# Kernel tuning notes

Hardware: AMD Instinct MI355X
Metric: run time of the kernel (lower is better)

## Reference

```python
import jax, jax.numpy as jnp
import numpy as np

EPS = 1e-5

def _ste(x, q):
    # straight-through estimator: forward = q, backward = identity
    return x + jax.lax.stop_gradient(q - x)

def quant_act_int4(x):
    # per-token absmax quantization to int4 range [-8, 7] (dequantized)
    s = jnp.clip(jnp.max(jnp.abs(x), axis=-1, keepdims=True), EPS, None) / 7.0
    q = jnp.clip(jnp.round(x / s), -8.0, 7.0) * s
    return _ste(x, q)

def ternary_weight(w):
    # absmean ternary quantization: scale = mean(|w|), w_q in {-1,0,+1} * scale
    scale = jnp.clip(jnp.mean(jnp.abs(w)), EPS, None)
    t = jnp.clip(jnp.round(w / scale), -1.0, 1.0)
    return _ste(w, t * scale)

def setup_inputs() -> dict:
    key = jax.random.key(0)
    kx, kw = jax.random.split(key)
    in_features, out_features = 4096, 16384
    x = jax.random.normal(kx, (4, 2048, in_features), dtype=jnp.float32)
    # kaiming_uniform_(a=sqrt(5)) -> U(-b, b), b = sqrt(6/((1+5)*fan_in)) = 1/sqrt(fan_in)
    bound = 1.0 / np.sqrt(in_features)
    latent_weight = jax.random.uniform(kw, (out_features, in_features), dtype=jnp.float32,
                                       minval=-bound, maxval=bound)
    return {"x": x, "latent_weight": latent_weight}

def reference(x, latent_weight):
    xq = quant_act_int4(x)                    # (B, S, in)
    w_eff = ternary_weight(latent_weight)     # (out, in)
    return jnp.einsum('bsi,oi->bso', xq, w_eff)
```

## Files before the change

### kernel.cpp

```cpp
#include <hip/hip_runtime.h>
#include <hip/hip_bf16.h>
#include <stdint.h>


#define K_DIM 4096
#define M_DIM 8192
#define N_DIM 16384

typedef int v4i __attribute__((ext_vector_type(4)));

typedef __attribute__((address_space(1))) void gvoid_t;
typedef __attribute__((address_space(3))) void lvoid_t;

__device__ __forceinline__ void gl_lds16(const void* g, void* l) {
    __builtin_amdgcn_global_load_lds((gvoid_t*)(void*)g, (lvoid_t*)l, 16, 0, 0);
}

__global__ __launch_bounds__(256) void wabs_partial_k(const float* __restrict__ w,
                                                      double* __restrict__ part) {
    const long n4 = (long)N_DIM * K_DIM / 4;
    long i = (long)blockIdx.x * blockDim.x + threadIdx.x;
    const long stride = (long)gridDim.x * blockDim.x;
    const float4* w4 = (const float4*)w;
    double s = 0.0;
    for (; i < n4; i += stride) {
        float4 v = w4[i];
        s += (double)fabsf(v.x);
        s += (double)fabsf(v.y);
        s += (double)fabsf(v.z);
        s += (double)fabsf(v.w);
    }
    __shared__ double red[256];
    const int tid = threadIdx.x;
    red[tid] = s;
    __syncthreads();
    for (int w2 = 128; w2 > 0; w2 >>= 1) {
        if (tid < w2) red[tid] += red[tid + w2];
        __syncthreads();
    }
    if (tid == 0) part[blockIdx.x] = red[0];
}

__global__ __launch_bounds__(256) void wscale_final_k(const double* __restrict__ part,
                                                      float* __restrict__ wscale) {
    __shared__ double red[256];
    const int tid = threadIdx.x;
    double s = 0.0;
    for (int i = tid; i < 1024; i += 256) s += part[i];
    red[tid] = s;
    __syncthreads();
    for (int w2 = 128; w2 > 0; w2 >>= 1) {
        if (tid < w2) red[tid] += red[tid + w2];
        __syncthreads();
    }
    if (tid == 0) {
        double mean = red[0] / (double)((long)N_DIM * K_DIM);
        *wscale = fmaxf((float)mean, 1e-5f);
    }
}

__global__ __launch_bounds__(256) void wquant_k(const float* __restrict__ w,
                                                signed char* __restrict__ qw,
                                                const float* __restrict__ wscale) {
    const float sc = *wscale;
    const long i = (long)blockIdx.x * 256 + threadIdx.x;
    const float4* w4 = (const float4*)(w + i * 16);
    union { signed char c[16]; int4 v; } u;
#pragma unroll
    for (int j = 0; j < 4; ++j) {
        float4 v = w4[j];
        u.c[j * 4 + 0] = (signed char)fminf(fmaxf(rintf(v.x / sc), -1.f), 1.f);
        u.c[j * 4 + 1] = (signed char)fminf(fmaxf(rintf(v.y / sc), -1.f), 1.f);
        u.c[j * 4 + 2] = (signed char)fminf(fmaxf(rintf(v.z / sc), -1.f), 1.f);
        u.c[j * 4 + 3] = (signed char)fminf(fmaxf(rintf(v.w / sc), -1.f), 1.f);
    }
    *(int4*)(qw + i * 16) = u.v;
}

__global__ __launch_bounds__(256) void xquant_k(const float* __restrict__ x,
                                                signed char* __restrict__ qx,
                                                float* __restrict__ sx,
                                                const float* __restrict__ wscale) {
    const int row = blockIdx.x;
    const int tid = threadIdx.x;
    const float4* xr = (const float4*)(x + (long)row * K_DIM) + tid * 4;
    float4 v[4];
    float am = 0.f;
#pragma unroll
    for (int j = 0; j < 4; ++j) {
        v[j] = xr[j];
        am = fmaxf(am, fmaxf(fmaxf(fabsf(v[j].x), fabsf(v[j].y)),
                             fmaxf(fabsf(v[j].z), fabsf(v[j].w))));
    }
#pragma unroll
    for (int off = 32; off > 0; off >>= 1) am = fmaxf(am, __shfl_down(am, off));
    __shared__ float wm[4];
    if ((tid & 63) == 0) wm[tid >> 6] = am;
    __syncthreads();
    am = fmaxf(fmaxf(wm[0], wm[1]), fmaxf(wm[2], wm[3]));
    const float s = fmaxf(am, 1e-5f) / 7.0f;
    union { signed char c[16]; int4 q; } u;
#pragma unroll
    for (int j = 0; j < 4; ++j) {
        u.c[j * 4 + 0] = (signed char)fminf(fmaxf(rintf(v[j].x / s), -8.f), 7.f);
        u.c[j * 4 + 1] = (signed char)fminf(fmaxf(rintf(v[j].y / s), -8.f), 7.f);
        u.c[j * 4 + 2] = (signed char)fminf(fmaxf(rintf(v[j].z / s), -8.f), 7.f);
        u.c[j * 4 + 3] = (signed char)fminf(fmaxf(rintf(v[j].w / s), -8.f), 7.f);
    }
    *(int4*)(qx + (long)row * K_DIM + tid * 16) = u.q;
    if (tid == 0) sx[row] = s * (*wscale);
}

__global__ __launch_bounds__(256) void gemm_k(const signed char* __restrict__ qx,
                                              const signed char* __restrict__ qw,
                                              const float* __restrict__ sx,
                                              float* __restrict__ out) {
    __shared__ signed char lA[128 * 64];
    __shared__ signed char lB[128 * 64];

    const int tid  = threadIdx.x;
    const int lane = tid & 63;
    const int wave = tid >> 6;
    const int m0 = blockIdx.x * 128;
    const int n0 = blockIdx.y * 128;
    const int wr = (wave >> 1) * 64;
    const int wc = (wave & 1) * 64;

    const int c0 = tid, c1 = tid + 256;
    const int r0 = c0 >> 2, r1 = c1 >> 2;
    const int g0 = ((c0 & 3) - ((r0 >> 1) & 3)) & 3;
    const int g1 = ((c1 & 3) - ((r1 >> 1) & 3)) & 3;
    const signed char* gA0 = qx + (long)(m0 + r0) * K_DIM + g0 * 16;
    const signed char* gA1 = qx + (long)(m0 + r1) * K_DIM + g1 * 16;
    const signed char* gB0 = qw + (long)(n0 + r0) * K_DIM + g0 * 16;
    const signed char* gB1 = qw + (long)(n0 + r1) * K_DIM + g1 * 16;
    signed char* lA0 = &lA[c0 * 16];
    signed char* lA1 = &lA[c1 * 16];
    signed char* lB0 = &lB[c0 * 16];
    signed char* lB1 = &lB[c1 * 16];

    const int fr = lane & 15;
    const int fq = lane >> 4;
    int offA[4], offB[4];
#pragma unroll
    for (int i = 0; i < 4; ++i) {
        int ra = wr + i * 16 + fr;
        offA[i] = ra * 64 + (((fq + (ra >> 1)) & 3) << 4);
        int rb = wc + i * 16 + fr;
        offB[i] = rb * 64 + (((fq + (rb >> 1)) & 3) << 4);
    }

    v4i acc[4][4];
#pragma unroll
    for (int i = 0; i < 4; ++i)
#pragma unroll
        for (int j = 0; j < 4; ++j) acc[i][j] = 0;

    for (int k0 = 0; k0 < K_DIM; k0 += 64) {
        __syncthreads();
        gl_lds16(gA0 + k0, lA0);
        gl_lds16(gA1 + k0, lA1);
        gl_lds16(gB0 + k0, lB0);
        gl_lds16(gB1 + k0, lB1);
        __syncthreads();

        v4i a[4], b[4];
#pragma unroll
        for (int i = 0; i < 4; ++i) a[i] = *(const v4i*)&lA[offA[i]];
#pragma unroll
        for (int i = 0; i < 4; ++i) b[i] = *(const v4i*)&lB[offB[i]];
#pragma unroll
        for (int i = 0; i < 4; ++i)
#pragma unroll
            for (int j = 0; j < 4; ++j)
                acc[i][j] = __builtin_amdgcn_mfma_i32_16x16x64_i8(a[i], b[j], acc[i][j], 0, 0, 0);
    }

#pragma unroll
    for (int i = 0; i < 4; ++i) {
#pragma unroll
        for (int r = 0; r < 4; ++r) {
            const int m = m0 + wr + i * 16 + fq * 4 + r;
            const float sm = sx[m];
#pragma unroll
            for (int j = 0; j < 4; ++j) {
                const int n = n0 + wc + j * 16 + fr;
                out[(long)m * N_DIM + n] = (float)acc[i][j][r] * sm;
            }
        }
    }
}

extern "C" void kernel_launch(void* const* d_in, const int* in_sizes, int n_in,
                              void* d_out, int out_size, void* d_ws, size_t ws_size,
                              hipStream_t stream) {
    const float* x = (const float*)d_in[0];
    const float* w = (const float*)d_in[1];
    float* out = (float*)d_out;
    char* ws = (char*)d_ws;

    double* part         = (double*)(ws);
    float*  wscale       = (float*)(ws + 8192);
    float*  sx           = (float*)(ws + 16384);
    signed char* qx      = (signed char*)(ws + 65536);
    signed char* qw      = (signed char*)(ws + 65536 + (size_t)33554432);

    wabs_partial_k<<<1024, 256, 0, stream>>>(w, part);
    wscale_final_k<<<1, 256, 0, stream>>>(part, wscale);
    wquant_k<<<16384, 256, 0, stream>>>(w, qw, wscale);
    xquant_k<<<8192, 256, 0, stream>>>(x, qx, sx, wscale);
    dim3 grid(M_DIM / 128, N_DIM / 128);
    gemm_k<<<grid, 256, 0, stream>>>(qx, qw, sx, out);
}
```

Baseline: 1.401 ms.

## Rework int8 GEMM into 256x256 tiles with a 4-stage LDS pipeline and XCD-aware mapping

The GEMM moves from 128x128 tiles with 256 threads and a single LDS buffer to 256x256 tiles with 512 threads and a four-slot LDS ring. Global-to-LDS loads for step t+2 are interleaved with the MFMA work, using explicit vmcnt waits, raw barriers and setprio. A swizzled 1D grid maps blocks per XCD so that tiles sharing operands land on the same L2. The quantization kernels are also changed to coalesced grid-stride access with 4-byte stores. The aim is to hide load latency and raise operand reuse, at the cost of 128KB of LDS per block and much higher register pressure.

```diff
diff --git a/kernel.cpp b/kernel.cpp
--- a/kernel.cpp
+++ b/kernel.cpp
@@ -1,5 +1,4 @@
 #include <hip/hip_runtime.h>
-#include <hip/hip_bf16.h>
 #include <stdint.h>
 
 
@@ -63,18 +62,20 @@
                                                 signed char* __restrict__ qw,
                                                 const float* __restrict__ wscale) {
     const float sc = *wscale;
-    const long i = (long)blockIdx.x * 256 + threadIdx.x;
-    const float4* w4 = (const float4*)(w + i * 16);
-    union { signed char c[16]; int4 v; } u;
-#pragma unroll
-    for (int j = 0; j < 4; ++j) {
-        float4 v = w4[j];
-        u.c[j * 4 + 0] = (signed char)fminf(fmaxf(rintf(v.x / sc), -1.f), 1.f);
-        u.c[j * 4 + 1] = (signed char)fminf(fmaxf(rintf(v.y / sc), -1.f), 1.f);
-        u.c[j * 4 + 2] = (signed char)fminf(fmaxf(rintf(v.z / sc), -1.f), 1.f);
-        u.c[j * 4 + 3] = (signed char)fminf(fmaxf(rintf(v.w / sc), -1.f), 1.f);
-    }
-    *(int4*)(qw + i * 16) = u.v;
+    const long n4 = (long)N_DIM * K_DIM / 4;
+    long i = (long)blockIdx.x * blockDim.x + threadIdx.x;
+    const long stride = (long)gridDim.x * blockDim.x;
+    const float4* w4 = (const float4*)w;
+    int* q4 = (int*)qw;
+    for (; i < n4; i += stride) {
+        float4 v = w4[i];
+        union { signed char c[4]; int u; } p;
+        p.c[0] = (signed char)fminf(fmaxf(rintf(v.x / sc), -1.f), 1.f);
+        p.c[1] = (signed char)fminf(fmaxf(rintf(v.y / sc), -1.f), 1.f);
+        p.c[2] = (signed char)fminf(fmaxf(rintf(v.z / sc), -1.f), 1.f);
+        p.c[3] = (signed char)fminf(fmaxf(rintf(v.w / sc), -1.f), 1.f);
+        q4[i] = p.u;
+    }
 }
 
 __global__ __launch_bounds__(256) void xquant_k(const float* __restrict__ x,
@@ -83,12 +84,12 @@
                                                 const float* __restrict__ wscale) {
     const int row = blockIdx.x;
     const int tid = threadIdx.x;
-    const float4* xr = (const float4*)(x + (long)row * K_DIM) + tid * 4;
+    const float4* xr = (const float4*)(x + (long)row * K_DIM);
     float4 v[4];
     float am = 0.f;
 #pragma unroll
     for (int j = 0; j < 4; ++j) {
-        v[j] = xr[j];
+        v[j] = xr[tid + j * 256];
         am = fmaxf(am, fmaxf(fmaxf(fabsf(v[j].x), fabsf(v[j].y)),
                              fmaxf(fabsf(v[j].z), fabsf(v[j].w))));
     }
@@ -99,94 +100,134 @@
     __syncthreads();
     am = fmaxf(fmaxf(wm[0], wm[1]), fmaxf(wm[2], wm[3]));
     const float s = fmaxf(am, 1e-5f) / 7.0f;
-    union { signed char c[16]; int4 q; } u;
+    int* qr = (int*)(qx + (long)row * K_DIM);
 #pragma unroll
     for (int j = 0; j < 4; ++j) {
-        u.c[j * 4 + 0] = (signed char)fminf(fmaxf(rintf(v[j].x / s), -8.f), 7.f);
-        u.c[j * 4 + 1] = (signed char)fminf(fmaxf(rintf(v[j].y / s), -8.f), 7.f);
-        u.c[j * 4 + 2] = (signed char)fminf(fmaxf(rintf(v[j].z / s), -8.f), 7.f);
-        u.c[j * 4 + 3] = (signed char)fminf(fmaxf(rintf(v[j].w / s), -8.f), 7.f);
-    }
-    *(int4*)(qx + (long)row * K_DIM + tid * 16) = u.q;
+        union { signed char c[4]; int u; } p;
+        p.c[0] = (signed char)fminf(fmaxf(rintf(v[j].x / s), -8.f), 7.f);
+        p.c[1] = (signed char)fminf(fmaxf(rintf(v[j].y / s), -8.f), 7.f);
+        p.c[2] = (signed char)fminf(fmaxf(rintf(v[j].z / s), -8.f), 7.f);
+        p.c[3] = (signed char)fminf(fmaxf(rintf(v[j].w / s), -8.f), 7.f);
+        qr[tid + j * 256] = p.u;
+    }
     if (tid == 0) sx[row] = s * (*wscale);
 }
 
-__global__ __launch_bounds__(256) void gemm_k(const signed char* __restrict__ qx,
+__global__ __launch_bounds__(512) void gemm_k(const signed char* __restrict__ qx,
                                               const signed char* __restrict__ qw,
                                               const float* __restrict__ sx,
                                               float* __restrict__ out) {
-    __shared__ signed char lA[128 * 64];
-    __shared__ signed char lB[128 * 64];
+    __shared__ __align__(16) signed char lds[4][32768];
 
     const int tid  = threadIdx.x;
     const int lane = tid & 63;
     const int wave = tid >> 6;
-    const int m0 = blockIdx.x * 128;
-    const int n0 = blockIdx.y * 128;
-    const int wr = (wave >> 1) * 64;
-    const int wc = (wave & 1) * 64;
-
-    const int c0 = tid, c1 = tid + 256;
-    const int r0 = c0 >> 2, r1 = c1 >> 2;
-    const int g0 = ((c0 & 3) - ((r0 >> 1) & 3)) & 3;
-    const int g1 = ((c1 & 3) - ((r1 >> 1) & 3)) & 3;
-    const signed char* gA0 = qx + (long)(m0 + r0) * K_DIM + g0 * 16;
-    const signed char* gA1 = qx + (long)(m0 + r1) * K_DIM + g1 * 16;
-    const signed char* gB0 = qw + (long)(n0 + r0) * K_DIM + g0 * 16;
-    const signed char* gB1 = qw + (long)(n0 + r1) * K_DIM + g1 * 16;
-    signed char* lA0 = &lA[c0 * 16];
-    signed char* lA1 = &lA[c1 * 16];
-    signed char* lB0 = &lB[c0 * 16];
-    signed char* lB1 = &lB[c1 * 16];
+    const int wm = wave >> 2;
+    const int wn = wave & 3;
+
+    const int bid = blockIdx.x;
+    const int xcd = bid & 7;
+    const int cid = bid >> 3;
+    const int mt  = (cid >> 1) & 31;
+    const int nt  = (xcd << 3) + ((cid >> 6) << 1) + (cid & 1);
+    const int m0 = mt << 8;
+    const int n0 = nt << 8;
+
+    const int r = tid >> 2;
+    const int g = ((tid & 3) - ((tid >> 3) & 3)) & 3;
+    const signed char* gA = qx + (long)(m0 + r) * K_DIM + (g << 4);
+    const signed char* gB = qw + (long)(n0 + r) * K_DIM + (g << 4);
+    const int oSA0 = tid << 4;
+    const int oSA1 = (tid << 4) + 8192;
+    const int oSB0 = (tid << 4) + 16384;
+    const int oSB1 = (tid << 4) + 24576;
 
     const int fr = lane & 15;
     const int fq = lane >> 4;
-    int offA[4], offB[4];
-#pragma unroll
-    for (int i = 0; i < 4; ++i) {
-        int ra = wr + i * 16 + fr;
+    int offA[8], offB[4];
+#pragma unroll
+    for (int i = 0; i < 8; ++i) {
+        const int ra = wm * 128 + i * 16 + fr;
         offA[i] = ra * 64 + (((fq + (ra >> 1)) & 3) << 4);
-        int rb = wc + i * 16 + fr;
-        offB[i] = rb * 64 + (((fq + (rb >> 1)) & 3) << 4);
-    }
-
-    v4i acc[4][4];
-#pragma unroll
-    for (int i = 0; i < 4; ++i)
+    }
+#pragma unroll
+    for (int j = 0; j < 4; ++j) {
+        const int rb = wn * 64 + j * 16 + fr;
+        offB[j] = 16384 + rb * 64 + (((fq + (rb >> 1)) & 3) << 4);
+    }
+
+    v4i acc[8][4];
+#pragma unroll
+    for (int i = 0; i < 8; ++i)
 #pragma unroll
         for (int j = 0; j < 4; ++j) acc[i][j] = 0;
 
-    for (int k0 = 0; k0 < K_DIM; k0 += 64) {
-        __syncthreads();
-        gl_lds16(gA0 + k0, lA0);
-        gl_lds16(gA1 + k0, lA1);
-        gl_lds16(gB0 + k0, lB0);
-        gl_lds16(gB1 + k0, lB1);
-        __syncthreads();
+    gl_lds16(gA,                      &lds[0][oSA0]);
+    gl_lds16(gA + 128 * K_DIM,        &lds[0][oSA1]);
+    gl_lds16(gB,                      &lds[0][oSB0]);
+    gl_lds16(gB + 128 * K_DIM,        &lds[0][oSB1]);
+    gl_lds16(gA + 64,                 &lds[1][oSA0]);
+    gl_lds16(gA + 128 * K_DIM + 64,   &lds[1][oSA1]);
+    gl_lds16(gB + 64,                 &lds[1][oSB0]);
+    gl_lds16(gB + 128 * K_DIM + 64,   &lds[1][oSB1]);
+
+    for (int t = 0; t < 64; ++t) {
+        if (t == 63) { asm volatile("s_waitcnt vmcnt(0)" ::: "memory"); }
+        else         { asm volatile("s_waitcnt vmcnt(4)" ::: "memory"); }
+        __builtin_amdgcn_s_barrier();
+
+        const signed char* cur = lds[t & 3];
+        signed char* nb = lds[(t + 2) & 3];
+        const long k2 = (long)(t + 2) << 6;
+        const bool st = (t < 62);
 
         v4i a[4], b[4];
-#pragma unroll
-        for (int i = 0; i < 4; ++i) a[i] = *(const v4i*)&lA[offA[i]];
-#pragma unroll
-        for (int i = 0; i < 4; ++i) b[i] = *(const v4i*)&lB[offB[i]];
+
+#pragma unroll
+        for (int j = 0; j < 4; ++j) b[j] = *(const v4i*)(cur + offB[j]);
+#pragma unroll
+        for (int i = 0; i < 4; ++i) a[i] = *(const v4i*)(cur + offA[i]);
+        if (st) {
+            gl_lds16(gA + k2,                 nb + oSA0);
+            gl_lds16(gA + 128 * K_DIM + k2,   nb + oSA1);
+        }
+        __builtin_amdgcn_s_barrier();
+        __builtin_amdgcn_s_setprio(1);
 #pragma unroll
         for (int i = 0; i < 4; ++i)
 #pragma unroll
             for (int j = 0; j < 4; ++j)
                 acc[i][j] = __builtin_amdgcn_mfma_i32_16x16x64_i8(a[i], b[j], acc[i][j], 0, 0, 0);
-    }
-
-#pragma unroll
-    for (int i = 0; i < 4; ++i) {
-#pragma unroll
-        for (int r = 0; r < 4; ++r) {
-            const int m = m0 + wr + i * 16 + fq * 4 + r;
+        __builtin_amdgcn_s_setprio(0);
+        __builtin_amdgcn_s_barrier();
+
+#pragma unroll
+        for (int i = 0; i < 4; ++i) a[i] = *(const v4i*)(cur + offA[4 + i]);
+        if (st) {
+            gl_lds16(gB + k2,                 nb + oSB0);
+            gl_lds16(gB + 128 * K_DIM + k2,   nb + oSB1);
+        }
+        __builtin_amdgcn_s_barrier();
+        __builtin_amdgcn_s_setprio(1);
+#pragma unroll
+        for (int i = 0; i < 4; ++i)
+#pragma unroll
+            for (int j = 0; j < 4; ++j)
+                acc[4 + i][j] = __builtin_amdgcn_mfma_i32_16x16x64_i8(a[i], b[j], acc[4 + i][j], 0, 0, 0);
+        __builtin_amdgcn_s_setprio(0);
+    }
+
+#pragma unroll
+    for (int i = 0; i < 8; ++i) {
+        const int mrow = m0 + wm * 128 + i * 16 + fq * 4;
+#pragma unroll
+        for (int rr = 0; rr < 4; ++rr) {
+            const int m = mrow + rr;
             const float sm = sx[m];
-#pragma unroll
-            for (int j = 0; j < 4; ++j) {
-                const int n = n0 + wc + j * 16 + fr;
-                out[(long)m * N_DIM + n] = (float)acc[i][j][r] * sm;
-            }
+            float* orow = out + (long)m * N_DIM + n0 + wn * 64 + fr;
+#pragma unroll
+            for (int j = 0; j < 4; ++j)
+                orow[j * 16] = (float)acc[i][j][rr] * sm;
         }
     }
 }
@@ -207,8 +248,7 @@
 
     wabs_partial_k<<<1024, 256, 0, stream>>>(w, part);
     wscale_final_k<<<1, 256, 0, stream>>>(part, wscale);
-    wquant_k<<<16384, 256, 0, stream>>>(w, qw, wscale);
+    wquant_k<<<2048, 256, 0, stream>>>(w, qw, wscale);
     xquant_k<<<8192, 256, 0, stream>>>(x, qx, sx, wscale);
-    dim3 grid(M_DIM / 128, N_DIM / 128);
-    gemm_k<<<grid, 256, 0, stream>>>(qx, qw, sx, out);
-}
+    gemm_k<<<2048, 512, 0, stream>>>(qx, qw, sx, out);
+}
```

Result: faster. 1.312 ms (-6.4%).
